# Kernel tuning notes

Measured on AMD Instinct MI355X. Metric: run time of the kernel, lower is better.

The kernel has to match this reference:

```python
import jax, jax.numpy as jnp
from jax import lax
import numpy as np

B, P, N = 4, 12000, 100   # batch, max_pillars, max_points_per_pillar
H, W = 108, 124           # pseudo-image size from forward()
DN = ('NCHW', 'HWIO', 'NCHW')


def _conv(x, k, b):
    y = lax.conv_general_dilated(x, k, (1, 1), 'SAME', dimension_numbers=DN)
    return y + b[None, :, None, None]


def _cbr(x, k, b, s, t):
    # Conv2d + folded BatchNorm2d (eval: per-channel scale/shift) + ReLU
    y = _conv(x, k, b)
    return jax.nn.relu(y * s[None, :, None, None] + t[None, :, None, None])


def _pool(x):
    return lax.reduce_window(x, -jnp.inf, lax.max, (1, 1, 2, 2), (1, 1, 2, 2), 'VALID')


def setup_inputs() -> dict:
    key = jax.random.key(0)
    ks = iter(jax.random.split(key, 64))
    d = {}
    d['pillars'] = jax.random.normal(next(ks), (B, P, N, 9), jnp.float32)

    def w(shape, scale=0.05):
        return jax.random.normal(next(ks), shape, jnp.float32) * scale

    d['w1'] = w((9, 64)); d['b1'] = w((64,))
    d['s1'] = 1.0 + w((64,)); d['t1'] = w((64,))
    d['w2'] = w((64, 64)); d['b2'] = w((64,))
    d['s2'] = 1.0 + w((64,)); d['t2'] = w((64,))
    chans = [(64, 64), (64, 64), (64, 128), (128, 128), (128, 256), (256, 256)]
    for i, (ci, co) in enumerate(chans, 1):
        d['ck%d' % i] = w((3, 3, ci, co)); d['cb%d' % i] = w((co,))
        d['cs%d' % i] = 1.0 + w((co,)); d['ct%d' % i] = w((co,))
    d['hk1'] = w((3, 3, 256, 256)); d['hb1'] = w((256,))
    d['hk2'] = w((1, 1, 256, 10)); d['hb2'] = w((10,))
    d['num_points'] = jax.random.randint(next(ks), (B, P), 0, 100, jnp.int32)
    return d


def reference(pillars, w1, b1, s1, t1, w2, b2, s2, t2,
              ck1, cb1, cs1, ct1, ck2, cb2, cs2, ct2,
              ck3, cb3, cs3, ct3, ck4, cb4, cs4, ct4,
              ck5, cb5, cs5, ct5, ck6, cb6, cs6, ct6,
              hk1, hb1, hk2, hb2, num_points):
    # pillar feature net: Linear+BN(folded)+ReLU x2, batched over all points  [B,P,N,9] -> [B,P,N,64]
    h = jax.nn.relu((pillars @ w1 + b1) * s1 + t1)
    h = jax.nn.relu((h @ w2 + b2) * s2 + t2)
    # masked segment-max over the variable-length point groups
    mask = jnp.arange(N)[None, None, :] < num_points[:, :, None]          # [B,P,N]
    neg = jnp.finfo(h.dtype).min
    feat = jnp.max(jnp.where(mask[..., None], h, neg), axis=2)            # [B,P,64]
    valid = num_points > 0
    feat = jnp.where(valid[..., None], feat, 0.0)
    cnt = jnp.maximum(jnp.sum(valid, axis=1), 1).astype(feat.dtype)       # [B]
    mean = jnp.sum(feat, axis=1) / cnt[:, None]                           # [B,64]
    # nearest-interpolate a 1x1 map to HxW == broadcast
    x = jnp.broadcast_to(mean[:, :, None, None], (pillars.shape[0], 64, H, W))
    # 2D backbone
    x = _cbr(x, ck1, cb1, cs1, ct1); x = _cbr(x, ck2, cb2, cs2, ct2); x = _pool(x)
    x = _cbr(x, ck3, cb3, cs3, ct3); x = _cbr(x, ck4, cb4, cs4, ct4); x = _pool(x)
    x = _cbr(x, ck5, cb5, cs5, ct5); x = _cbr(x, ck6, cb6, cs6, ct6)
    # detection head
    y = jax.nn.relu(_conv(x, hk1, hb1))
    return _conv(y, hk2, hb2)   # [B, num_classes+7=10, 27, 31]
```

## Files before the change

### kernel.cpp

```cpp
#include <hip/hip_runtime.h>

typedef __bf16 vbf8 __attribute__((ext_vector_type(8)));
typedef unsigned short us8 __attribute__((ext_vector_type(8)));
typedef float f32x4 __attribute__((ext_vector_type(4)));
typedef float f32x4u __attribute__((ext_vector_type(4), aligned(4)));

#define NBLK 32

__device__ __forceinline__ int caseof(int h, int H, int e) {
  if (h < 0 || h >= H) return -1;
  if (h < e) return h;
  if (h >= H - e) return h - (H - 1) + 2 * e;
  return e;
}
__device__ __forceinline__ int repof(int i, int H, int eo) {
  return (i <= eo) ? i : H - 1 - 2 * eo + i;
}

__device__ __forceinline__ vbf8 max8(vbf8 a, vbf8 b) {
  us8 ua = __builtin_bit_cast(us8, a), ub = __builtin_bit_cast(us8, b);
  us8 o;
#pragma unroll
  for (int e = 0; e < 8; ++e) o[e] = ua[e] > ub[e] ? ua[e] : ub[e];
  return __builtin_bit_cast(vbf8, o);
}

__device__ __forceinline__ void gridbar(int* bar) {
  __syncthreads();
  if (threadIdx.x == 0) {
    int* cnt = bar; int* gen = bar + 1;
    int g = __hip_atomic_load(gen, __ATOMIC_RELAXED, __HIP_MEMORY_SCOPE_SYSTEM);
    if (__hip_atomic_fetch_add(cnt, 1, __ATOMIC_ACQ_REL, __HIP_MEMORY_SCOPE_AGENT) == NBLK - 1) {
      __hip_atomic_store(cnt, 0, __ATOMIC_RELAXED, __HIP_MEMORY_SCOPE_AGENT);
      __hip_atomic_store(gen, g + 1, __ATOMIC_RELEASE, __HIP_MEMORY_SCOPE_SYSTEM);
    } else {
      while (__hip_atomic_load(gen, __ATOMIC_RELAXED, __HIP_MEMORY_SCOPE_SYSTEM) == g)
        __builtin_amdgcn_s_sleep(4);
      __builtin_amdgcn_fence(__ATOMIC_ACQUIRE, "agent");
    }
  }
  __syncthreads();
}

__global__ __launch_bounds__(256) void prep_kernel(
    const float* __restrict__ k1, const float* __restrict__ k2,
    const float* __restrict__ k3, const float* __restrict__ k4,
    const float* __restrict__ k5, const float* __restrict__ k6,
    const float* __restrict__ kh, __bf16* __restrict__ wT,
    const float* __restrict__ w1, const float* __restrict__ b1,
    const float* __restrict__ s1, const float* __restrict__ t1,
    const float* __restrict__ w2, const float* __restrict__ b2,
    const float* __restrict__ s2, const float* __restrict__ t2,
    __bf16* __restrict__ wfrag, float* __restrict__ be2f,
    __bf16* __restrict__ zbuf, int* __restrict__ bar) {
  __shared__ float tile[64][65];
  if (blockIdx.x == 432) {
    int l = threadIdx.x;
    if (l < 64) {
      int s = l & 15, g = l >> 4;
#pragma unroll
      for (int m = 0; m < 4; ++m) {
        int c = 32 * (m & 1) + 8 * (s >> 2) + 4 * (m >> 1) + (s & 3);
#pragma unroll
        for (int e = 0; e < 8; ++e) {
          int k = g * 8 + e;
          float v = 0.f;
          if (k < 9)       v = w1[k * 64 + c] * s1[c];
          else if (k == 9) v = fmaf(b1[c], s1[c], t1[c]);
          wfrag[(m * 64 + l) * 8 + e] = (__bf16)v;
        }
        int co = s + 16 * m;
#pragma unroll
        for (int e = 0; e < 8; ++e) {
          int k = g * 8 + e;
          wfrag[((4 + m) * 64 + l) * 8 + e] = (__bf16)(w2[k * 64 + co] * s2[co]);
          wfrag[((8 + m) * 64 + l) * 8 + e] = (__bf16)(w2[(32 + k) * 64 + co] * s2[co]);
        }
        be2f[m * 64 + l] = fmaf(b2[co], s2[co], t2[co]);
      }
    } else if (l >= 64 && l < 128) {
      int z = l - 64;
#pragma unroll
      for (int i = 0; i < 4; ++i) zbuf[z * 4 + i] = (__bf16)0.f;
    } else if (l == 128) {
      bar[0] = 0; bar[1] = 0;
    }
    return;
  }
  const int tCI[7]    = {64, 64, 64, 128, 128, 256, 256};
  const int tCO[7]    = {64, 64, 128, 128, 256, 256, 256};
  const int tOFF[7]   = {0, 36864, 73728, 147456, 294912, 589824, 1179648};
  const int tTILES[7] = {9, 9, 18, 36, 72, 144, 144};
  int bid = blockIdx.x;
  int ti = 0, acc = 0;
  while (ti < 6 && bid >= acc + tTILES[ti]) { acc += tTILES[ti]; ++ti; }
  int lt = bid - acc;
  int CI = tCI[ti], CO = tCO[ti];
  const float* src;
  if (ti == 0) src = k1; else if (ti == 1) src = k2; else if (ti == 2) src = k3;
  else if (ti == 3) src = k4; else if (ti == 4) src = k5; else if (ti == 5) src = k6;
  else src = kh;
  int cot = CO / 64, tpt = (CI / 64) * cot;
  int tap = lt / tpt; int r2 = lt - tap * tpt;
  int ci0 = (r2 / cot) * 64, co0 = (r2 % cot) * 64;
  const float* sp = src + (size_t)(tap * CI + ci0) * CO + co0;
  int t = threadIdx.x;
  int lr = t >> 6, lc = t & 63;
#pragma unroll
  for (int rr = 0; rr < 64; rr += 4)
    tile[rr + lr][lc] = sp[(size_t)(rr + lr) * CO + lc];
  __syncthreads();
  __bf16* dst = wT + tOFF[ti] + ((size_t)tap * CO + co0) * CI + ci0;
#pragma unroll
  for (int rr = 0; rr < 64; rr += 4)
    dst[(size_t)(rr + lr) * CI + lc] = (__bf16)tile[lc][rr + lr];
}

__global__ __launch_bounds__(256) void pillar_kernel(
    const float* __restrict__ pil, const int* __restrict__ npt,
    const __bf16* __restrict__ wfrag, const float* __restrict__ be2f,
    float* __restrict__ partial, int* __restrict__ pcnt)
{
  __shared__ float redf[4][64];
  __shared__ int redc[4];
  const int tid = threadIdx.x;
  const int wv = tid >> 6, lane = tid & 63;
  const int s = lane & 15, g = lane >> 4;
  const int wid = blockIdx.x * 4 + wv;
  const int b = wid / 6000;
  const int p0 = (wid - b * 6000) * 2;

  vbf8 w1f[4], w2f0[4], w2f1[4];
  float be2[4];
#pragma unroll
  for (int m = 0; m < 4; ++m) {
    w1f[m]  = *(const vbf8*)(wfrag + ((0 + m) * 64 + lane) * 8);
    w2f0[m] = *(const vbf8*)(wfrag + ((4 + m) * 64 + lane) * 8);
    w2f1[m] = *(const vbf8*)(wfrag + ((8 + m) * 64 + lane) * 8);
    be2[m] = be2f[m * 64 + lane];
  }

  float fsum[4] = {0.f, 0.f, 0.f, 0.f};
  int cnt = 0;

  for (int i = 0; i < 2; ++i) {
    int pidx = b * 12000 + p0 + i;
    int np = npt[pidx];
    if (np <= 0) continue;
    ++cnt;
    float feat[4][4];
#pragma unroll
    for (int n = 0; n < 4; ++n)
#pragma unroll
      for (int r = 0; r < 4; ++r) feat[n][r] = 0.f;

    int ngrp = (np + 15) >> 4;
    const float* pbase = pil + (size_t)pidx * 900;
    const float* pp0 = pbase + s * 9;
    f32x4u lo = *(const f32x4u*)pp0;
    f32x4u hi = *(const f32x4u*)(pp0 + 4);
    float v8 = pp0[8];
    for (int grp = 0; grp < ngrp; ++grp) {
      int g2 = min(grp + 1, ngrp - 1);
      int ptn = min(g2 * 16 + s, 99);
      const float* ppn = pbase + ptn * 9;
      f32x4u nlo = *(const f32x4u*)ppn;
      f32x4u nhi = *(const f32x4u*)(ppn + 4);
      float nv8 = ppn[8];

      vbf8 b1f;
      b1f[0] = (__bf16)(g == 0 ? lo[0] : (g == 1 ? v8 : 0.f));
      b1f[1] = (__bf16)(g == 0 ? lo[1] : (g == 1 ? 1.0f : 0.f));
      b1f[2] = (__bf16)(g == 0 ? lo[2] : 0.f);
      b1f[3] = (__bf16)(g == 0 ? lo[3] : 0.f);
      b1f[4] = (__bf16)(g == 0 ? hi[0] : 0.f);
      b1f[5] = (__bf16)(g == 0 ? hi[1] : 0.f);
      b1f[6] = (__bf16)(g == 0 ? hi[2] : 0.f);
      b1f[7] = (__bf16)(g == 0 ? hi[3] : 0.f);

      const f32x4 z = {0.f, 0.f, 0.f, 0.f};
      f32x4 d1[4];
#pragma unroll
      for (int m = 0; m < 4; ++m)
        d1[m] = __builtin_amdgcn_mfma_f32_16x16x32_bf16(w1f[m], b1f, z, 0, 0, 0);

      vbf8 a2f0, a2f1;
#pragma unroll
      for (int r = 0; r < 4; ++r) {
        a2f0[r]     = (__bf16)fmaxf(d1[0][r], 0.f);
        a2f1[r]     = (__bf16)fmaxf(d1[1][r], 0.f);
        a2f0[4 + r] = (__bf16)fmaxf(d1[2][r], 0.f);
        a2f1[4 + r] = (__bf16)fmaxf(d1[3][r], 0.f);
      }

      f32x4 d2[4];
#pragma unroll
      for (int n = 0; n < 4; ++n) {
        f32x4 cb = {be2[n], be2[n], be2[n], be2[n]};
        d2[n] = __builtin_amdgcn_mfma_f32_16x16x32_bf16(a2f0, w2f0[n], cb, 0, 0, 0);
        d2[n] = __builtin_amdgcn_mfma_f32_16x16x32_bf16(a2f1, w2f1[n], d2[n], 0, 0, 0);
      }
      if (((grp + 1) << 4) <= np) {
#pragma unroll
        for (int n = 0; n < 4; ++n)
#pragma unroll
          for (int r = 0; r < 4; ++r) feat[n][r] = fmaxf(feat[n][r], d2[n][r]);
      } else {
#pragma unroll
        for (int n = 0; n < 4; ++n)
#pragma unroll
          for (int r = 0; r < 4; ++r) {
            float vv = (grp * 16 + 4 * g + r < np) ? d2[n][r] : 0.f;
            feat[n][r] = fmaxf(feat[n][r], vv);
          }
      }
      lo = nlo; hi = nhi; v8 = nv8;
    }
#pragma unroll
    for (int n = 0; n < 4; ++n) {
      float m = fmaxf(fmaxf(feat[n][0], feat[n][1]), fmaxf(feat[n][2], feat[n][3]));
      m = fmaxf(m, __shfl_xor(m, 16));
      m = fmaxf(m, __shfl_xor(m, 32));
      fsum[n] += m;
    }
  }
  if (g == 0) {
#pragma unroll
    for (int n = 0; n < 4; ++n) redf[wv][s + 16 * n] = fsum[n];
  }
  if (lane == 0) redc[wv] = cnt;
  __syncthreads();
  if (tid < 64) {
    float tot = redf[0][tid] + redf[1][tid] + redf[2][tid] + redf[3][tid];
    partial[blockIdx.x * 64 + tid] = tot;
    if (tid == 0) pcnt[blockIdx.x] = redc[0] + redc[1] + redc[2] + redc[3];
  }
}

template <int CI, int CO, int H, int EIN, bool POOL, bool HAS_BN, bool OUT_F32>
__device__ __forceinline__ void caseconv_dev(
    int wid0, const __bf16* __restrict__ xin, const __bf16* __restrict__ wt,
    const float* __restrict__ cb, const float* __restrict__ cs,
    const float* __restrict__ ct, __bf16* __restrict__ yout,
    float* __restrict__ yf32, const __bf16* __restrict__ zbuf)
{
  constexpr int EV   = POOL ? (EIN + 1) / 2 : EIN;
  constexpr int EOUT = EV + 1;
  constexpr int NBI  = 2 * EIN + 1;
  constexpr int HX   = POOL ? 2 * H : H;
  constexpr int NBO  = 2 * EOUT + 1;
  constexpr int M    = NBO * NBO * 4;
  constexpr int NT   = CO / 16;
  constexpr int KC   = CI / 32;
  constexpr int MT   = (M + 31) / 32;
  const int lane = threadIdx.x & 63;
  const int s = lane & 15, g = lane >> 4;

  for (int wid = wid0; wid < MT * NT; wid += NBLK * 4) {
    const int nt = wid % NT, mt = wid / NT;
    int reph[2], repw[2], bsel[2];
#pragma unroll
    for (int mf = 0; mf < 2; ++mf) {
      int m = mt * 32 + mf * 16 + s; if (m >= M) m = M - 1;
      bsel[mf] = m & 3; int q = m >> 2;
      int bw = q % NBO, bh = q / NBO;
      reph[mf] = repof(bh, H, EOUT); repw[mf] = repof(bw, H, EOUT);
    }

    f32x4 acc0 = {0.f, 0.f, 0.f, 0.f}, acc1 = {0.f, 0.f, 0.f, 0.f};
#pragma unroll
    for (int tap = 0; tap < 9; ++tap) {
      const int dh = tap / 3, dw = tap % 3;
      const __bf16* wtap = wt + ((size_t)tap * CO + nt * 16) * CI + 8 * g;
      const __bf16* base[2][POOL ? 4 : 1];
#pragma unroll
      for (int mf = 0; mf < 2; ++mf) {
        int vh = reph[mf] + dh - 1, vw = repw[mf] + dw - 1;
        if constexpr (POOL) {
          bool valid = (vh >= 0) && (vh < H) && (vw >= 0) && (vw < H);
          int h0 = 0, h1 = 0, w0 = 0, w1 = 0;
          if (valid) {
            h0 = caseof(2 * vh, HX, EIN); h1 = caseof(2 * vh + 1, HX, EIN);
            w0 = caseof(2 * vw, HX, EIN); w1 = caseof(2 * vw + 1, HX, EIN);
          }
          base[mf][0] = valid ? xin + (size_t)((h0 * NBI + w0) * 4 + bsel[mf]) * CI : zbuf;
          base[mf][1] = valid ? xin + (size_t)((h0 * NBI + w1) * 4 + bsel[mf]) * CI : zbuf;
          base[mf][2] = valid ? xin + (size_t)((h1 * NBI + w0) * 4 + bsel[mf]) * CI : zbuf;
          base[mf][3] = valid ? xin + (size_t)((h1 * NBI + w1) * 4 + bsel[mf]) * CI : zbuf;
        } else {
          int jh = caseof(vh, H, EIN), jw = caseof(vw, H, EIN);
          bool v = (jh >= 0) && (jw >= 0);
          base[mf][0] = v ? xin + (size_t)((jh * NBI + jw) * 4 + bsel[mf]) * CI : zbuf;
        }
      }
#pragma unroll
      for (int ck = 0; ck < KC; ++ck) {
        vbf8 a0, a1;
        if constexpr (POOL) {
          a0 = max8(max8(*(const vbf8*)(base[0][0] + ck * 32 + 8 * g),
                         *(const vbf8*)(base[0][1] + ck * 32 + 8 * g)),
                    max8(*(const vbf8*)(base[0][2] + ck * 32 + 8 * g),
                         *(const vbf8*)(base[0][3] + ck * 32 + 8 * g)));
          a1 = max8(max8(*(const vbf8*)(base[1][0] + ck * 32 + 8 * g),
                         *(const vbf8*)(base[1][1] + ck * 32 + 8 * g)),
                    max8(*(const vbf8*)(base[1][2] + ck * 32 + 8 * g),
                         *(const vbf8*)(base[1][3] + ck * 32 + 8 * g)));
        } else {
          a0 = *(const vbf8*)(base[0][0] + ck * 32 + 8 * g);
          a1 = *(const vbf8*)(base[1][0] + ck * 32 + 8 * g);
        }
        vbf8 bb = *(const vbf8*)(wtap + (size_t)s * CI + ck * 32);
        acc0 = __builtin_amdgcn_mfma_f32_16x16x32_bf16(a0, bb, acc0, 0, 0, 0);
        acc1 = __builtin_amdgcn_mfma_f32_16x16x32_bf16(a1, bb, acc1, 0, 0, 0);
      }
    }

    int co = nt * 16 + s;
    float sc, sh;
    if (HAS_BN) { sc = cs[co]; sh = fmaf(cb[co], sc, ct[co]); }
    else        { sc = 1.f;    sh = cb[co]; }
#pragma unroll
    for (int mf = 0; mf < 2; ++mf) {
      f32x4 acc = mf ? acc1 : acc0;
#pragma unroll
      for (int r = 0; r < 4; ++r) {
        int m = mt * 32 + mf * 16 + 4 * g + r;
        if (m < M) {
          float v = fmaxf(fmaf(acc[r], sc, sh), 0.f);
          if constexpr (OUT_F32) yf32[(size_t)m * CO + co] = v;
          else                   yout[(size_t)m * CO + co] = (__bf16)v;
        }
      }
    }
  }
}

__global__ __launch_bounds__(256) void backbone_kernel(
    const float* __restrict__ ppart, const int* __restrict__ pcnt,
    __bf16* __restrict__ X0, __bf16* __restrict__ X2, __bf16* __restrict__ X3,
    __bf16* __restrict__ X4, __bf16* __restrict__ X5, __bf16* __restrict__ X6,
    float* __restrict__ XH,
    const __bf16* wt1, const __bf16* wt2, const __bf16* wt3, const __bf16* wt4,
    const __bf16* wt5, const __bf16* wt6, const __bf16* wth,
    const float* cb1, const float* cs1, const float* ct1,
    const float* cb2, const float* cs2, const float* ct2,
    const float* cb3, const float* cs3, const float* ct3,
    const float* cb4, const float* cs4, const float* ct4,
    const float* cb5, const float* cs5, const float* ct5,
    const float* cb6, const float* cs6, const float* ct6,
    const float* hb1, const float* hk2, const float* hb2,
    const __bf16* __restrict__ zbuf, int* __restrict__ bar,
    float* __restrict__ out)
{
  __shared__ __bf16 ldsX1[36 * 64];
  __shared__ __bf16 zp[64];
  const int tid = threadIdx.x;
  const int wv = tid >> 6, lane = tid & 63;
  const int s = lane & 15, g = lane >> 4;
  const int wid = blockIdx.x * 4 + wv;
  const int gtid = blockIdx.x * 256 + tid;

  if (blockIdx.x < 4) {
    int b = blockIdx.x;
    int c = tid & 63, q = tid >> 6;
    float sum = 0.f;
    for (int w = q; w < 1500; w += 4) sum += ppart[(b * 1500 + w) * 64 + c];
    int cl = 0;
    for (int w = tid; w < 1500; w += 256) cl += pcnt[b * 1500 + w];
    __shared__ float sh[256];
    __shared__ int shc[256];
    sh[tid] = sum; shc[tid] = cl;
    __syncthreads();
    for (int o = 128; o > 0; o >>= 1) {
      if (tid < o) shc[tid] += shc[tid + o];
      __syncthreads();
    }
    if (tid < 64) {
      float tot = sh[tid] + sh[tid + 64] + sh[tid + 128] + sh[tid + 192];
      X0[b * 64 + tid] = (__bf16)(tot / (float)(shc[0] > 0 ? shc[0] : 1));
    }
  }
  if (tid < 64) zp[tid] = (__bf16)0.f;
  gridbar(bar);

  if (blockIdx.x < 4) {
    for (int t8 = wv; t8 < 8; t8 += 4) {
      int nt = t8 & 3, mt = t8 >> 2;
      int reph[2], repw[2], bsel[2];
#pragma unroll
      for (int mf = 0; mf < 2; ++mf) {
        int m = mt * 32 + mf * 16 + s; if (m >= 36) m = 35;
        bsel[mf] = m & 3; int q = m >> 2;
        int bw = q % 3, bh = q / 3;
        reph[mf] = repof(bh, 64, 1); repw[mf] = repof(bw, 64, 1);
      }
      f32x4 acc0 = {0.f, 0.f, 0.f, 0.f}, acc1 = {0.f, 0.f, 0.f, 0.f};
#pragma unroll
      for (int tap = 0; tap < 9; ++tap) {
        int dh = tap / 3, dw = tap % 3;
        const __bf16* wtap = wt1 + ((size_t)tap * 64 + nt * 16) * 64 + 8 * g;
        const __bf16* pa[2];
#pragma unroll
        for (int mf = 0; mf < 2; ++mf) {
          int vh = reph[mf] + dh - 1, vw = repw[mf] + dw - 1;
          bool v = (vh >= 0) && (vh < 64) && (vw >= 0) && (vw < 64);
          pa[mf] = v ? X0 + bsel[mf] * 64 : zbuf;
        }
#pragma unroll
        for (int ck = 0; ck < 2; ++ck) {
          vbf8 a0 = *(const vbf8*)(pa[0] + ck * 32 + 8 * g);
          vbf8 a1 = *(const vbf8*)(pa[1] + ck * 32 + 8 * g);
          vbf8 bb = *(const vbf8*)(wtap + (size_t)s * 64 + ck * 32);
          acc0 = __builtin_amdgcn_mfma_f32_16x16x32_bf16(a0, bb, acc0, 0, 0, 0);
          acc1 = __builtin_amdgcn_mfma_f32_16x16x32_bf16(a1, bb, acc1, 0, 0, 0);
        }
      }
      int co = nt * 16 + s;
      float sc = cs1[co], shv = fmaf(cb1[co], sc, ct1[co]);
#pragma unroll
      for (int mf = 0; mf < 2; ++mf) {
        f32x4 acc = mf ? acc1 : acc0;
#pragma unroll
        for (int r = 0; r < 4; ++r) {
          int m = mt * 32 + mf * 16 + 4 * g + r;
          if (m < 36)
            ldsX1[m * 64 + co] = (__bf16)fmaxf(fmaf(acc[r], sc, shv), 0.f);
        }
      }
    }
    __syncthreads();
    {
      int t16 = blockIdx.x * 4 + wv;
      int nt = t16 & 3, mt = t16 >> 2;
      int reph[2], repw[2], bsel[2];
#pragma unroll
      for (int mf = 0; mf < 2; ++mf) {
        int m = mt * 32 + mf * 16 + s; if (m >= 100) m = 99;
        bsel[mf] = m & 3; int q = m >> 2;
        int bw = q % 5, bh = q / 5;
        reph[mf] = repof(bh, 64, 2); repw[mf] = repof(bw, 64, 2);
      }
      f32x4 acc0 = {0.f, 0.f, 0.f, 0.f}, acc1 = {0.f, 0.f, 0.f, 0.f};
#pragma unroll
      for (int tap = 0; tap < 9; ++tap) {
        int dh = tap / 3, dw = tap % 3;
        const __bf16* wtap = wt2 + ((size_t)tap * 64 + nt * 16) * 64 + 8 * g;
        const __bf16* pa[2];
#pragma unroll
        for (int mf = 0; mf < 2; ++mf) {
          int jh = caseof(reph[mf] + dh - 1, 64, 1);
          int jw = caseof(repw[mf] + dw - 1, 64, 1);
          bool v = (jh >= 0) && (jw >= 0);
          pa[mf] = v ? ldsX1 + ((jh * 3 + jw) * 4 + bsel[mf]) * 64 : zp;
        }
#pragma unroll
        for (int ck = 0; ck < 2; ++ck) {
          vbf8 a0 = *(const vbf8*)(pa[0] + ck * 32 + 8 * g);
          vbf8 a1 = *(const vbf8*)(pa[1] + ck * 32 + 8 * g);
          vbf8 bb = *(const vbf8*)(wtap + (size_t)s * 64 + ck * 32);
          acc0 = __builtin_amdgcn_mfma_f32_16x16x32_bf16(a0, bb, acc0, 0, 0, 0);
          acc1 = __builtin_amdgcn_mfma_f32_16x16x32_bf16(a1, bb, acc1, 0, 0, 0);
        }
      }
      int co = nt * 16 + s;
      float sc = cs2[co], shv = fmaf(cb2[co], sc, ct2[co]);
#pragma unroll
      for (int mf = 0; mf < 2; ++mf) {
        f32x4 acc = mf ? acc1 : acc0;
#pragma unroll
        for (int r = 0; r < 4; ++r) {
          int m = mt * 32 + mf * 16 + 4 * g + r;
          if (m < 100)
            X2[(size_t)m * 64 + co] = (__bf16)fmaxf(fmaf(acc[r], sc, shv), 0.f);
        }
      }
    }
  }
  gridbar(bar);
  caseconv_dev<64, 128, 32, 2, true, true, false>(wid, X2, wt3, cb3, cs3, ct3, X3, nullptr, zbuf);
  gridbar(bar);
  caseconv_dev<128, 128, 32, 2, false, true, false>(wid, X3, wt4, cb4, cs4, ct4, X4, nullptr, zbuf);
  gridbar(bar);
  caseconv_dev<128, 256, 16, 3, true, true, false>(wid, X4, wt5, cb5, cs5, ct5, X5, nullptr, zbuf);
  gridbar(bar);
  caseconv_dev<256, 256, 16, 3, false, true, false>(wid, X5, wt6, cb6, cs6, ct6, X6, nullptr, zbuf);
  gridbar(bar);
  caseconv_dev<256, 256, 16, 4, false, false, true>(wid, X6, wth, hb1, nullptr, nullptr, nullptr, XH, zbuf);
  gridbar(bar);
  for (int idx = gtid; idx < 4 * 10 * 27 * 31; idx += NBLK * 256) {
    int c = idx % 31;
    int r = (idx / 31) % 27;
    int ch = (idx / (31 * 27)) % 10;
    int b = idx / (31 * 27 * 10);
    int rr = (r <= 7) ? r : ((r >= 20) ? r - 11 : 7);
    int cc = (c <= 7) ? c : ((c >= 24) ? c - 15 : 7);
    int ph = caseof(rr, 16, 5), pw = caseof(cc, 16, 5);
    const float* xr = XH + (size_t)((ph * 11 + pw) * 4 + b) * 256;
    float a0 = 0.f, a1 = 0.f, a2 = 0.f, a3 = 0.f;
#pragma unroll 4
    for (int ci = 0; ci < 256; ci += 4) {
      float4 in4 = *(const float4*)(xr + ci);
      a0 = fmaf(in4.x, hk2[(ci + 0) * 10 + ch], a0);
      a1 = fmaf(in4.y, hk2[(ci + 1) * 10 + ch], a1);
      a2 = fmaf(in4.z, hk2[(ci + 2) * 10 + ch], a2);
      a3 = fmaf(in4.w, hk2[(ci + 3) * 10 + ch], a3);
    }
    out[idx] = (a0 + a1) + (a2 + a3) + hb2[ch];
  }
}

extern "C" void kernel_launch(void* const* d_in, const int* in_sizes, int n_in,
                              void* d_out, int out_size, void* d_ws, size_t ws_size,
                              hipStream_t stream) {
  (void)in_sizes; (void)n_in; (void)out_size; (void)ws_size;
  const float* pillars = (const float*)d_in[0];
  const float* w1 = (const float*)d_in[1];
  const float* b1 = (const float*)d_in[2];
  const float* s1 = (const float*)d_in[3];
  const float* t1 = (const float*)d_in[4];
  const float* w2 = (const float*)d_in[5];
  const float* b2 = (const float*)d_in[6];
  const float* s2 = (const float*)d_in[7];
  const float* t2 = (const float*)d_in[8];
  const float* ck[6], *cbv[6], *csv[6], *ctv[6];
  for (int i = 0; i < 6; ++i) {
    ck[i]  = (const float*)d_in[9 + i * 4];
    cbv[i] = (const float*)d_in[10 + i * 4];
    csv[i] = (const float*)d_in[11 + i * 4];
    ctv[i] = (const float*)d_in[12 + i * 4];
  }
  const float* hk1 = (const float*)d_in[33];
  const float* hb1 = (const float*)d_in[34];
  const float* hk2 = (const float*)d_in[35];
  const float* hb2 = (const float*)d_in[36];
  const int* num_points = (const int*)d_in[37];
  float* out = (float*)d_out;

  char* wsb = (char*)d_ws;
  size_t off = 0;
  auto alloc = [&](size_t n) { char* p = wsb + off; off = (off + n + 255) & ~(size_t)255; return p; };
  float*  ppart = (float*)alloc(1536000);
  int*    pcnt  = (int*)alloc(24000);
  __bf16* wfrag = (__bf16*)alloc(12288);
  float*  be2f  = (float*)alloc(1024);
  __bf16* wT    = (__bf16*)alloc(3538944);
  __bf16* zbuf  = (__bf16*)alloc(512);
  int*    bar   = (int*)alloc(256);
  __bf16* X0    = (__bf16*)alloc(512);
  __bf16* X2    = (__bf16*)alloc(12800);
  __bf16* X3    = (__bf16*)alloc(25600);
  __bf16* X4    = (__bf16*)alloc(50176);
  __bf16* X5    = (__bf16*)alloc(100352);
  __bf16* X6    = (__bf16*)alloc(165888);
  float*  XH    = (float*)alloc(495616);

  __bf16* wt1 = wT + 0;       __bf16* wt2 = wT + 36864;
  __bf16* wt3 = wT + 73728;   __bf16* wt4 = wT + 147456;
  __bf16* wt5 = wT + 294912;  __bf16* wt6 = wT + 589824;
  __bf16* wth = wT + 1179648;

  prep_kernel<<<433, 256, 0, stream>>>(ck[0], ck[1], ck[2], ck[3], ck[4], ck[5],
                                       hk1, wT, w1, b1, s1, t1, w2, b2, s2, t2,
                                       wfrag, be2f, zbuf, bar);
  pillar_kernel<<<6000, 256, 0, stream>>>(pillars, num_points, wfrag, be2f,
                                          ppart, pcnt);
  backbone_kernel<<<NBLK, 256, 0, stream>>>(
      ppart, pcnt, X0, X2, X3, X4, X5, X6, XH,
      wt1, wt2, wt3, wt4, wt5, wt6, wth,
      cbv[0], csv[0], ctv[0], cbv[1], csv[1], ctv[1],
      cbv[2], csv[2], ctv[2], cbv[3], csv[3], ctv[3],
      cbv[4], csv[4], ctv[4], cbv[5], csv[5], ctv[5],
      hb1, hk2, hb2, zbuf, bar, out);
}
```

Before: 414.4 us.

## Fuse weight prep into pillar kernel and pre-swizzle conv weights to MFMA fragments

Result: faster. 398.1 us (-3.9%).

```diff
diff --git a/kernel.cpp b/kernel.cpp
--- a/kernel.cpp
+++ b/kernel.cpp
@@ -29,116 +29,106 @@
   __syncthreads();
   if (threadIdx.x == 0) {
     int* cnt = bar; int* gen = bar + 1;
-    int g = __hip_atomic_load(gen, __ATOMIC_RELAXED, __HIP_MEMORY_SCOPE_SYSTEM);
+    int g = __hip_atomic_load(gen, __ATOMIC_RELAXED, __HIP_MEMORY_SCOPE_AGENT);
     if (__hip_atomic_fetch_add(cnt, 1, __ATOMIC_ACQ_REL, __HIP_MEMORY_SCOPE_AGENT) == NBLK - 1) {
       __hip_atomic_store(cnt, 0, __ATOMIC_RELAXED, __HIP_MEMORY_SCOPE_AGENT);
-      __hip_atomic_store(gen, g + 1, __ATOMIC_RELEASE, __HIP_MEMORY_SCOPE_SYSTEM);
+      __hip_atomic_store(gen, g + 1, __ATOMIC_RELEASE, __HIP_MEMORY_SCOPE_AGENT);
     } else {
-      while (__hip_atomic_load(gen, __ATOMIC_RELAXED, __HIP_MEMORY_SCOPE_SYSTEM) == g)
-        __builtin_amdgcn_s_sleep(4);
-      __builtin_amdgcn_fence(__ATOMIC_ACQUIRE, "agent");
+      while (__hip_atomic_load(gen, __ATOMIC_RELAXED, __HIP_MEMORY_SCOPE_AGENT) == g)
+        __builtin_amdgcn_s_sleep(8);
+      __threadfence();
     }
   }
   __syncthreads();
 }
 
-__global__ __launch_bounds__(256) void prep_kernel(
+__global__ __launch_bounds__(256) void pillar_kernel(
+    const float* __restrict__ pil, const int* __restrict__ npt,
+    const float* __restrict__ w1, const float* __restrict__ b1,
+    const float* __restrict__ s1, const float* __restrict__ t1,
+    const float* __restrict__ w2, const float* __restrict__ b2,
+    const float* __restrict__ s2, const float* __restrict__ t2,
     const float* __restrict__ k1, const float* __restrict__ k2,
     const float* __restrict__ k3, const float* __restrict__ k4,
     const float* __restrict__ k5, const float* __restrict__ k6,
     const float* __restrict__ kh, __bf16* __restrict__ wT,
-    const float* __restrict__ w1, const float* __restrict__ b1,
-    const float* __restrict__ s1, const float* __restrict__ t1,
-    const float* __restrict__ w2, const float* __restrict__ b2,
-    const float* __restrict__ s2, const float* __restrict__ t2,
-    __bf16* __restrict__ wfrag, float* __restrict__ be2f,
-    __bf16* __restrict__ zbuf, int* __restrict__ bar) {
-  __shared__ float tile[64][65];
-  if (blockIdx.x == 432) {
-    int l = threadIdx.x;
-    if (l < 64) {
-      int s = l & 15, g = l >> 4;
-#pragma unroll
-      for (int m = 0; m < 4; ++m) {
-        int c = 32 * (m & 1) + 8 * (s >> 2) + 4 * (m >> 1) + (s & 3);
-#pragma unroll
-        for (int e = 0; e < 8; ++e) {
-          int k = g * 8 + e;
-          float v = 0.f;
-          if (k < 9)       v = w1[k * 64 + c] * s1[c];
-          else if (k == 9) v = fmaf(b1[c], s1[c], t1[c]);
-          wfrag[(m * 64 + l) * 8 + e] = (__bf16)v;
-        }
-        int co = s + 16 * m;
-#pragma unroll
-        for (int e = 0; e < 8; ++e) {
-          int k = g * 8 + e;
-          wfrag[((4 + m) * 64 + l) * 8 + e] = (__bf16)(w2[k * 64 + co] * s2[co]);
-          wfrag[((8 + m) * 64 + l) * 8 + e] = (__bf16)(w2[(32 + k) * 64 + co] * s2[co]);
-        }
-        be2f[m * 64 + l] = fmaf(b2[co], s2[co], t2[co]);
-      }
-    } else if (l >= 64 && l < 128) {
-      int z = l - 64;
-#pragma unroll
-      for (int i = 0; i < 4; ++i) zbuf[z * 4 + i] = (__bf16)0.f;
-    } else if (l == 128) {
-      bar[0] = 0; bar[1] = 0;
-    }
-    return;
-  }
-  const int tCI[7]    = {64, 64, 64, 128, 128, 256, 256};
-  const int tCO[7]    = {64, 64, 128, 128, 256, 256, 256};
-  const int tOFF[7]   = {0, 36864, 73728, 147456, 294912, 589824, 1179648};
-  const int tTILES[7] = {9, 9, 18, 36, 72, 144, 144};
-  int bid = blockIdx.x;
-  int ti = 0, acc = 0;
-  while (ti < 6 && bid >= acc + tTILES[ti]) { acc += tTILES[ti]; ++ti; }
-  int lt = bid - acc;
-  int CI = tCI[ti], CO = tCO[ti];
-  const float* src;
-  if (ti == 0) src = k1; else if (ti == 1) src = k2; else if (ti == 2) src = k3;
-  else if (ti == 3) src = k4; else if (ti == 4) src = k5; else if (ti == 5) src = k6;
-  else src = kh;
-  int cot = CO / 64, tpt = (CI / 64) * cot;
-  int tap = lt / tpt; int r2 = lt - tap * tpt;
-  int ci0 = (r2 / cot) * 64, co0 = (r2 % cot) * 64;
-  const float* sp = src + (size_t)(tap * CI + ci0) * CO + co0;
-  int t = threadIdx.x;
-  int lr = t >> 6, lc = t & 63;
-#pragma unroll
-  for (int rr = 0; rr < 64; rr += 4)
-    tile[rr + lr][lc] = sp[(size_t)(rr + lr) * CO + lc];
-  __syncthreads();
-  __bf16* dst = wT + tOFF[ti] + ((size_t)tap * CO + co0) * CI + ci0;
-#pragma unroll
-  for (int rr = 0; rr < 64; rr += 4)
-    dst[(size_t)(rr + lr) * CI + lc] = (__bf16)tile[lc][rr + lr];
-}
-
-__global__ __launch_bounds__(256) void pillar_kernel(
-    const float* __restrict__ pil, const int* __restrict__ npt,
-    const __bf16* __restrict__ wfrag, const float* __restrict__ be2f,
+    __bf16* __restrict__ zbuf, int* __restrict__ bar,
     float* __restrict__ partial, int* __restrict__ pcnt)
 {
+  __shared__ float tile[64][65];
   __shared__ float redf[4][64];
   __shared__ int redc[4];
   const int tid = threadIdx.x;
   const int wv = tid >> 6, lane = tid & 63;
   const int s = lane & 15, g = lane >> 4;
+
+  if (blockIdx.x == 0) {
+    zbuf[tid] = (__bf16)0.f;
+    if (tid < 2) bar[tid] = 0;
+  }
+
+  if (blockIdx.x < 432) {
+    const int tCI[7]    = {64, 64, 64, 128, 128, 256, 256};
+    const int tCO[7]    = {64, 64, 128, 128, 256, 256, 256};
+    const int tOFF[7]   = {0, 36864, 73728, 147456, 294912, 589824, 1179648};
+    const int tTILES[7] = {9, 9, 18, 36, 72, 144, 144};
+    int bid = blockIdx.x;
+    int ti = 0, acc = 0;
+    while (ti < 6 && bid >= acc + tTILES[ti]) { acc += tTILES[ti]; ++ti; }
+    int lt = bid - acc;
+    int CI = tCI[ti], CO = tCO[ti];
+    const float* src;
+    if (ti == 0) src = k1; else if (ti == 1) src = k2; else if (ti == 2) src = k3;
+    else if (ti == 3) src = k4; else if (ti == 4) src = k5; else if (ti == 5) src = k6;
+    else src = kh;
+    int cot = CO / 64, tpt = (CI / 64) * cot;
+    int tap = lt / tpt; int r2 = lt - tap * tpt;
+    int ci0 = (r2 / cot) * 64, co0 = (r2 % cot) * 64;
+    const float* sp = src + (size_t)(tap * CI + ci0) * CO + co0;
+    int lr = tid >> 6, lc = tid & 63;
+#pragma unroll
+    for (int rr = 0; rr < 64; rr += 4)
+      tile[rr + lr][lc] = sp[(size_t)(rr + lr) * CO + lc];
+    __syncthreads();
+    __bf16* dstL = wT + tOFF[ti];
+    int NT = CO >> 4, KCw = CI >> 5;
+#pragma unroll
+    for (int rr = 0; rr < 64; rr += 4) {
+      int co = co0 + rr + lr;
+      int ci = ci0 + lc;
+      int nt = co >> 4, ss = co & 15;
+      int ck = ci >> 5, gg = (ci >> 3) & 3, ee = ci & 7;
+      size_t off = ((((size_t)tap * NT + nt) * KCw + ck) * 64 + gg * 16 + ss) * 8 + ee;
+      dstL[off] = (__bf16)tile[lc][rr + lr];
+    }
+  }
+
+  vbf8 w1f[4], w2f0[4], w2f1[4];
+  float be2[4];
+#pragma unroll
+  for (int m = 0; m < 4; ++m) {
+    int c = 32 * (m & 1) + 8 * (s >> 2) + 4 * (m >> 1) + (s & 3);
+#pragma unroll
+    for (int e = 0; e < 8; ++e) {
+      int k = g * 8 + e;
+      float v = 0.f;
+      if (k < 9)       v = w1[k * 64 + c] * s1[c];
+      else if (k == 9) v = fmaf(b1[c], s1[c], t1[c]);
+      w1f[m][e] = (__bf16)v;
+    }
+    int co = s + 16 * m;
+#pragma unroll
+    for (int e = 0; e < 8; ++e) {
+      int k = g * 8 + e;
+      w2f0[m][e] = (__bf16)(w2[k * 64 + co] * s2[co]);
+      w2f1[m][e] = (__bf16)(w2[(32 + k) * 64 + co] * s2[co]);
+    }
+    be2[m] = fmaf(b2[co], s2[co], t2[co]);
+  }
+
   const int wid = blockIdx.x * 4 + wv;
   const int b = wid / 6000;
   const int p0 = (wid - b * 6000) * 2;
-
-  vbf8 w1f[4], w2f0[4], w2f1[4];
-  float be2[4];
-#pragma unroll
-  for (int m = 0; m < 4; ++m) {
-    w1f[m]  = *(const vbf8*)(wfrag + ((0 + m) * 64 + lane) * 8);
-    w2f0[m] = *(const vbf8*)(wfrag + ((4 + m) * 64 + lane) * 8);
-    w2f1[m] = *(const vbf8*)(wfrag + ((8 + m) * 64 + lane) * 8);
-    be2[m] = be2f[m * 64 + lane];
-  }
 
   float fsum[4] = {0.f, 0.f, 0.f, 0.f};
   int cnt = 0;
@@ -239,7 +229,7 @@
 
 template <int CI, int CO, int H, int EIN, bool POOL, bool HAS_BN, bool OUT_F32>
 __device__ __forceinline__ void caseconv_dev(
-    int wid0, const __bf16* __restrict__ xin, const __bf16* __restrict__ wt,
+    int wid0, const __bf16* __restrict__ xin, const __bf16* __restrict__ wp,
     const float* __restrict__ cb, const float* __restrict__ cs,
     const float* __restrict__ ct, __bf16* __restrict__ yout,
     float* __restrict__ yf32, const __bf16* __restrict__ zbuf)
@@ -271,7 +261,6 @@
 #pragma unroll
     for (int tap = 0; tap < 9; ++tap) {
       const int dh = tap / 3, dw = tap % 3;
-      const __bf16* wtap = wt + ((size_t)tap * CO + nt * 16) * CI + 8 * g;
       const __bf16* base[2][POOL ? 4 : 1];
 #pragma unroll
       for (int mf = 0; mf < 2; ++mf) {
@@ -309,7 +298,7 @@
           a0 = *(const vbf8*)(base[0][0] + ck * 32 + 8 * g);
           a1 = *(const vbf8*)(base[1][0] + ck * 32 + 8 * g);
         }
-        vbf8 bb = *(const vbf8*)(wtap + (size_t)s * CI + ck * 32);
+        vbf8 bb = *(const vbf8*)(wp + (((size_t)tap * NT + nt) * KC + ck) * 512 + lane * 8);
         acc0 = __builtin_amdgcn_mfma_f32_16x16x32_bf16(a0, bb, acc0, 0, 0, 0);
         acc1 = __builtin_amdgcn_mfma_f32_16x16x32_bf16(a1, bb, acc1, 0, 0, 0);
       }
@@ -354,6 +343,8 @@
 {
   __shared__ __bf16 ldsX1[36 * 64];
   __shared__ __bf16 zp[64];
+  __shared__ f32x4 mvec[16 * 16];
+  __shared__ int mcnt[256];
   const int tid = threadIdx.x;
   const int wv = tid >> 6, lane = tid & 63;
   const int s = lane & 15, g = lane >> 4;
@@ -362,28 +353,34 @@
 
   if (blockIdx.x < 4) {
     int b = blockIdx.x;
-    int c = tid & 63, q = tid >> 6;
-    float sum = 0.f;
-    for (int w = q; w < 1500; w += 4) sum += ppart[(b * 1500 + w) * 64 + c];
+    int c4 = tid & 15, wr = tid >> 4;
+    f32x4 sum = {0.f, 0.f, 0.f, 0.f};
+    for (int w = wr; w < 1500; w += 16)
+      sum += *(const f32x4u*)(ppart + (size_t)(b * 1500 + w) * 64 + c4 * 4);
+    mvec[wr * 16 + c4] = sum;
     int cl = 0;
     for (int w = tid; w < 1500; w += 256) cl += pcnt[b * 1500 + w];
-    __shared__ float sh[256];
-    __shared__ int shc[256];
-    sh[tid] = sum; shc[tid] = cl;
+    mcnt[tid] = cl;
     __syncthreads();
     for (int o = 128; o > 0; o >>= 1) {
-      if (tid < o) shc[tid] += shc[tid + o];
+      if (tid < o) mcnt[tid] += mcnt[tid + o];
       __syncthreads();
     }
-    if (tid < 64) {
-      float tot = sh[tid] + sh[tid + 64] + sh[tid + 128] + sh[tid + 192];
-      X0[b * 64 + tid] = (__bf16)(tot / (float)(shc[0] > 0 ? shc[0] : 1));
+    for (int o = 8; o > 0; o >>= 1) {
+      if (wr < o) mvec[wr * 16 + c4] += mvec[(wr + o) * 16 + c4];
+      __syncthreads();
+    }
+    if (tid < 16) {
+      f32x4 tot = mvec[tid];
+      float inv = 1.f / (float)(mcnt[0] > 0 ? mcnt[0] : 1);
+#pragma unroll
+      for (int e = 0; e < 4; ++e) X0[b * 64 + tid * 4 + e] = (__bf16)(tot[e] * inv);
     }
   }
   if (tid < 64) zp[tid] = (__bf16)0.f;
   gridbar(bar);
 
-  if (blockIdx.x < 4) {
+  {
     for (int t8 = wv; t8 < 8; t8 += 4) {
       int nt = t8 & 3, mt = t8 >> 2;
       int reph[2], repw[2], bsel[2];
@@ -398,7 +395,6 @@
 #pragma unroll
       for (int tap = 0; tap < 9; ++tap) {
         int dh = tap / 3, dw = tap % 3;
-        const __bf16* wtap = wt1 + ((size_t)tap * 64 + nt * 16) * 64 + 8 * g;
         const __bf16* pa[2];
 #pragma unroll
         for (int mf = 0; mf < 2; ++mf) {
@@ -410,7 +406,7 @@
         for (int ck = 0; ck < 2; ++ck) {
           vbf8 a0 = *(const vbf8*)(pa[0] + ck * 32 + 8 * g);
           vbf8 a1 = *(const vbf8*)(pa[1] + ck * 32 + 8 * g);
-          vbf8 bb = *(const vbf8*)(wtap + (size_t)s * 64 + ck * 32);
+          vbf8 bb = *(const vbf8*)(wt1 + (((size_t)tap * 4 + nt) * 2 + ck) * 512 + lane * 8);
           acc0 = __builtin_amdgcn_mfma_f32_16x16x32_bf16(a0, bb, acc0, 0, 0, 0);
           acc1 = __builtin_amdgcn_mfma_f32_16x16x32_bf16(a1, bb, acc1, 0, 0, 0);
         }
@@ -429,7 +425,7 @@
       }
     }
     __syncthreads();
-    {
+    if (blockIdx.x < 4) {
       int t16 = blockIdx.x * 4 + wv;
       int nt = t16 & 3, mt = t16 >> 2;
       int reph[2], repw[2], bsel[2];
@@ -444,7 +440,6 @@
 #pragma unroll
       for (int tap = 0; tap < 9; ++tap) {
         int dh = tap / 3, dw = tap % 3;
-        const __bf16* wtap = wt2 + ((size_t)tap * 64 + nt * 16) * 64 + 8 * g;
         const __bf16* pa[2];
 #pragma unroll
         for (int mf = 0; mf < 2; ++mf) {
@@ -457,7 +452,7 @@
         for (int ck = 0; ck < 2; ++ck) {
           vbf8 a0 = *(const vbf8*)(pa[0] + ck * 32 + 8 * g);
           vbf8 a1 = *(const vbf8*)(pa[1] + ck * 32 + 8 * g);
-          vbf8 bb = *(const vbf8*)(wtap + (size_t)s * 64 + ck * 32);
+          vbf8 bb = *(const vbf8*)(wt2 + (((size_t)tap * 4 + nt) * 2 + ck) * 512 + lane * 8);
           acc0 = __builtin_amdgcn_mfma_f32_16x16x32_bf16(a0, bb, acc0, 0, 0, 0);
           acc1 = __builtin_amdgcn_mfma_f32_16x16x32_bf16(a1, bb, acc1, 0, 0, 0);
         }
@@ -541,8 +536,6 @@
   auto alloc = [&](size_t n) { char* p = wsb + off; off = (off + n + 255) & ~(size_t)255; return p; };
   float*  ppart = (float*)alloc(1536000);
   int*    pcnt  = (int*)alloc(24000);
-  __bf16* wfrag = (__bf16*)alloc(12288);
-  float*  be2f  = (float*)alloc(1024);
   __bf16* wT    = (__bf16*)alloc(3538944);
   __bf16* zbuf  = (__bf16*)alloc(512);
   int*    bar   = (int*)alloc(256);
@@ -559,11 +552,9 @@
   __bf16* wt5 = wT + 294912;  __bf16* wt6 = wT + 589824;
   __bf16* wth = wT + 1179648;
 
-  prep_kernel<<<433, 256, 0, stream>>>(ck[0], ck[1], ck[2], ck[3], ck[4], ck[5],
-                                       hk1, wT, w1, b1, s1, t1, w2, b2, s2, t2,
-                                       wfrag, be2f, zbuf, bar);
-  pillar_kernel<<<6000, 256, 0, stream>>>(pillars, num_points, wfrag, be2f,
-                                          ppart, pcnt);
+  pillar_kernel<<<6000, 256, 0, stream>>>(
+      pillars, num_points, w1, b1, s1, t1, w2, b2, s2, t2,
+      ck[0], ck[1], ck[2], ck[3], ck[4], ck[5], hk1, wT, zbuf, bar, ppart, pcnt);
   backbone_kernel<<<NBLK, 256, 0, stream>>>(
       ppart, pcnt, X0, X2, X3, X4, X5, X6, XH,
       wt1, wt2, wt3, wt4, wt5, wt6, wth,
```
